# Optimization experiments

Hardware: AMD Instinct MI355X
Metric: run time of the kernel (lower is better)

## Reference

```python
import jax, jax.numpy as jnp
import numpy as np
import math

B, S, E = 2, 2048, 1024
H, HD = 16, 64
FF = 4 * E
EPS = float(jnp.finfo(jnp.float32).eps)  # torch nn.RMSNorm default eps


def setup_inputs() -> dict:
    key = jax.random.key(0)
    ks = jax.random.split(key, 20)
    sd = 0.02
    inp = {
        "x": jax.random.normal(ks[0], (B, S, E), jnp.float32),
        "wq": jax.random.normal(ks[1], (E, H * HD), jnp.float32) * sd,
        "bq": jnp.zeros((H * HD,), jnp.float32),
        "wk": jax.random.normal(ks[2], (E, HD), jnp.float32) * sd,
        "bk": jnp.zeros((HD,), jnp.float32),
        "wv": jax.random.normal(ks[3], (E, HD), jnp.float32) * sd,
        "bv": jnp.zeros((HD,), jnp.float32),
        "wo": jax.random.normal(ks[4], (H * HD, E), jnp.float32) * sd,
        "bo": jnp.zeros((E,), jnp.float32),
        "wg": jax.random.normal(ks[5], (E, FF), jnp.float32) * sd,
        "bg": jnp.zeros((FF,), jnp.float32),
        "wu": jax.random.normal(ks[6], (E, FF), jnp.float32) * sd,
        "bu": jnp.zeros((FF,), jnp.float32),
        "wd": jax.random.normal(ks[7], (FF, E), jnp.float32) * sd,
        "bd": jnp.zeros((E,), jnp.float32),
        "g1": jnp.ones((E,), jnp.float32),
        "g2": jnp.ones((E,), jnp.float32),
    }
    return inp


def rmsnorm(x, g):
    ms = jnp.mean(jnp.square(x), axis=-1, keepdims=True)
    return x * jax.lax.rsqrt(ms + EPS) * g


def apply_rope(t):
    # t: [B, H, S, D]; llama-style rotate-half, theta=10000, start_pos=0
    d = t.shape[-1]
    half = d // 2
    inv_freq = 1.0 / (10000.0 ** (jnp.arange(half, dtype=jnp.float32) / half))
    pos = jnp.arange(t.shape[2], dtype=jnp.float32)
    ang = pos[:, None] * inv_freq[None, :]  # [S, half]
    cos, sin = jnp.cos(ang), jnp.sin(ang)
    t1, t2 = t[..., :half], t[..., half:]
    return jnp.concatenate([t1 * cos - t2 * sin, t1 * sin + t2 * cos], axis=-1)


def decoder_fwd(x, wq, bq, wk, bk, wv, bv, wo, bo, wg, bg, wu, bu, wd, bd, g1, g2):
    residual = x
    h = rmsnorm(x, g1)
    # MQA projections: H query heads, 1 shared K/V head
    q = (h @ wq + bq).reshape(B, S, H, HD).transpose(0, 2, 1, 3)  # [B,H,S,D]
    k = (h @ wk + bk)[:, None]                                    # [B,1,S,D]
    v = (h @ wv + bv)                                             # [B,S,D]
    q = apply_rope(q)
    k = apply_rope(k)[:, 0]                                       # [B,S,D]
    scores = jnp.einsum("bhqd,bkd->bhqk", q, k) / math.sqrt(HD)
    causal = jnp.tril(jnp.ones((S, S), dtype=bool))
    scores = jnp.where(causal, scores, -jnp.inf)
    attn = jax.nn.softmax(scores, axis=-1)
    out = jnp.einsum("bhqk,bkd->bhqd", attn, v)
    out = out.transpose(0, 2, 1, 3).reshape(B, S, H * HD)
    x = (out @ wo + bo) + residual
    residual = x
    h = rmsnorm(x, g2)
    gated = jax.nn.gelu(h @ wg + bg, approximate=False)  # torch GELU is exact erf
    up = h @ wu + bu
    x = (up * gated) @ wd + bd
    return x + residual


def reference(x, wq, bq, wk, bk, wv, bv, wo, bo, wg, bg, wu, bu, wd, bd, g1, g2):
    return decoder_fwd(x, wq, bq, wk, bk, wv, bv, wo, bo, wg, bg, wu, bu, wd, bd, g1, g2)
```

## Files before the change

kernel.cpp:

```cpp
#include <hip/hip_runtime.h>
#include <hip/hip_bf16.h>
#include <math.h>

#define BB 2
#define SS 2048
#define EE 1024
#define HH 16
#define HD 64
#define FFF 4096
#define MROWS (BB * SS)
#define EPS_F 1.1920929e-7f
#define NQKV 1152

typedef __hip_bfloat16 bf16;
typedef __attribute__((ext_vector_type(8))) short short8;
typedef __attribute__((ext_vector_type(4))) short short4v;
typedef __attribute__((ext_vector_type(4))) float floatx4;

typedef const __attribute__((address_space(1))) void* gas_t;
typedef __attribute__((address_space(3))) void* las_t;

#define BAR __builtin_amdgcn_s_barrier()
#define WLG do { asm volatile("s_waitcnt lgkmcnt(0)" ::: "memory"); \
                 __builtin_amdgcn_sched_barrier(0); } while (0)
#define VMC(N) asm volatile("s_waitcnt vmcnt(" #N ")" ::: "memory")

__global__ __launch_bounds__(256) void rmsnorm_kernel(const float* __restrict__ x,
                                                      const float* __restrict__ g,
                                                      bf16* __restrict__ out,
                                                      int cols) {
    int row = blockIdx.x;
    const float* xr = x + (size_t)row * cols;
    float ss = 0.0f;
    for (int c = threadIdx.x; c < cols; c += 256) {
        float v = xr[c];
        ss += v * v;
    }
    for (int off = 32; off > 0; off >>= 1) ss += __shfl_xor(ss, off, 64);
    __shared__ float red[4];
    int wave = threadIdx.x >> 6;
    if ((threadIdx.x & 63) == 0) red[wave] = ss;
    __syncthreads();
    float tot = red[0] + red[1] + red[2] + red[3];
    float rs = rsqrtf(tot / (float)cols + EPS_F);
    bf16* orow = out + (size_t)row * cols;
    for (int c = threadIdx.x; c < cols; c += 256) {
        orow[c] = __float2bfloat16(xr[c] * rs * g[c]);
    }
}

__global__ __launch_bounds__(256) void transpose_cast_kernel(const float* __restrict__ W,
                                                             bf16* __restrict__ Wt,
                                                             int K, int N) {
    __shared__ float t[32][33];
    int n0 = blockIdx.x * 32, k0 = blockIdx.y * 32;
    int tx = threadIdx.x & 31, ty = threadIdx.x >> 5;
#pragma unroll
    for (int i = 0; i < 4; ++i) {
        int kk = ty + i * 8;
        t[kk][tx] = W[(size_t)(k0 + kk) * N + n0 + tx];
    }
    __syncthreads();
#pragma unroll
    for (int i = 0; i < 4; ++i) {
        int nn = ty + i * 8;
        Wt[(size_t)(n0 + nn) * K + k0 + tx] = __float2bfloat16(t[tx][nn]);
    }
}

__global__ __launch_bounds__(256) void pack_bqkv_kernel(const float* __restrict__ bq,
                                                        const float* __restrict__ bk,
                                                        const float* __restrict__ bv,
                                                        float* __restrict__ bqkv) {
    int t = blockIdx.x * 256 + threadIdx.x;
    if (t >= NQKV) return;
    float v;
    if (t < 1024)      v = bq[t];
    else if (t < 1088) v = bk[t - 1024];
    else               v = bv[t - 1088];
    bqkv[t] = v;
}

#define GK 64

__global__ __launch_bounds__(256) void gemm_qkv_kernel(
        const bf16* __restrict__ A, const bf16* __restrict__ Bt,
        const float* __restrict__ bias,
        bf16* __restrict__ qout, float* __restrict__ kvout, int K) {
    __shared__ short As[128 * GK];
    __shared__ short Bs[128 * GK];
    int tid = threadIdx.x;
    int wave = tid >> 6, lane = tid & 63;
    int wm = (wave >> 1) * 64, wn = (wave & 1) * 64;
    int row0 = blockIdx.y * 128, col0 = blockIdx.x * 128;
    int lr = lane & 15, lq = lane >> 4;

    int srow = wave * 32 + (lane >> 3);
    int scol = (lane & 7) * 8;
    const bf16* Abase = A + (size_t)(row0 + srow) * K + scol;
    const bf16* Bbase = Bt + (size_t)(col0 + srow) * K + scol;

    floatx4 acc[4][4];
#pragma unroll
    for (int mi = 0; mi < 4; ++mi)
#pragma unroll
        for (int ni = 0; ni < 4; ++ni)
            acc[mi][ni] = (floatx4){0.f, 0.f, 0.f, 0.f};

    for (int k0 = 0; k0 < K; k0 += GK) {
        __syncthreads();
#pragma unroll
        for (int c = 0; c < 4; ++c) {
            __builtin_amdgcn_global_load_lds(
                (gas_t)(Abase + (size_t)(c * 8) * K + k0),
                (las_t)&As[(wave * 32 + c * 8) * GK], 16, 0, 0);
            __builtin_amdgcn_global_load_lds(
                (gas_t)(Bbase + (size_t)(c * 8) * K + k0),
                (las_t)&Bs[(wave * 32 + c * 8) * GK], 16, 0, 0);
        }
        __syncthreads();
#pragma unroll
        for (int ks = 0; ks < GK; ks += 32) {
            short8 af[4], bfr[4];
#pragma unroll
            for (int mi = 0; mi < 4; ++mi)
                af[mi] = *(const short8*)&As[(wm + mi * 16 + lr) * GK + ks + lq * 8];
#pragma unroll
            for (int ni = 0; ni < 4; ++ni)
                bfr[ni] = *(const short8*)&Bs[(wn + ni * 16 + lr) * GK + ks + lq * 8];
#pragma unroll
            for (int mi = 0; mi < 4; ++mi)
#pragma unroll
                for (int ni = 0; ni < 4; ++ni)
                    acc[mi][ni] = __builtin_amdgcn_mfma_f32_16x16x32_bf16(
                        af[mi], bfr[ni], acc[mi][ni], 0, 0, 0);
        }
    }

#pragma unroll
    for (int mi = 0; mi < 4; ++mi) {
#pragma unroll
        for (int ni = 0; ni < 4; ++ni) {
            int gc = col0 + wn + ni * 16 + lr;
            float bv = bias[gc];
#pragma unroll
            for (int r = 0; r < 4; ++r) {
                int gr = row0 + wm + mi * 16 + lq * 4 + r;
                float c = acc[mi][ni][r] + bv;
                if (gc < 1024) qout[(size_t)gr * 1024 + gc] = __float2bfloat16(c);
                else           kvout[(size_t)gr * 128 + (gc - 1024)] = c;
            }
        }
    }
}

__global__ __launch_bounds__(256) void gemm_n128_kernel(
        const bf16* __restrict__ A, const bf16* __restrict__ Bt,
        const float* __restrict__ bias, const float* __restrict__ aux,
        float* __restrict__ C, int N, int K) {
    __shared__ short As[128 * GK];
    __shared__ short Bs[128 * GK];
    int tid = threadIdx.x;
    int wave = tid >> 6, lane = tid & 63;
    int wm = (wave >> 1) * 64, wn = (wave & 1) * 64;
    int row0 = blockIdx.y * 128, col0 = blockIdx.x * 128;
    int lr = lane & 15, lq = lane >> 4;

    int srow = wave * 32 + (lane >> 3);
    int scol = (lane & 7) * 8;
    const bf16* Abase = A + (size_t)(row0 + srow) * K + scol;
    const bf16* Bbase = Bt + (size_t)(col0 + srow) * K + scol;

    floatx4 acc[4][4];
#pragma unroll
    for (int mi = 0; mi < 4; ++mi)
#pragma unroll
        for (int ni = 0; ni < 4; ++ni)
            acc[mi][ni] = (floatx4){0.f, 0.f, 0.f, 0.f};

    for (int k0 = 0; k0 < K; k0 += GK) {
        __syncthreads();
#pragma unroll
        for (int c = 0; c < 4; ++c) {
            __builtin_amdgcn_global_load_lds(
                (gas_t)(Abase + (size_t)(c * 8) * K + k0),
                (las_t)&As[(wave * 32 + c * 8) * GK], 16, 0, 0);
            __builtin_amdgcn_global_load_lds(
                (gas_t)(Bbase + (size_t)(c * 8) * K + k0),
                (las_t)&Bs[(wave * 32 + c * 8) * GK], 16, 0, 0);
        }
        __syncthreads();
#pragma unroll
        for (int ks = 0; ks < GK; ks += 32) {
            short8 af[4], bfr[4];
#pragma unroll
            for (int mi = 0; mi < 4; ++mi)
                af[mi] = *(const short8*)&As[(wm + mi * 16 + lr) * GK + ks + lq * 8];
#pragma unroll
            for (int ni = 0; ni < 4; ++ni)
                bfr[ni] = *(const short8*)&Bs[(wn + ni * 16 + lr) * GK + ks + lq * 8];
#pragma unroll
            for (int mi = 0; mi < 4; ++mi)
#pragma unroll
                for (int ni = 0; ni < 4; ++ni)
                    acc[mi][ni] = __builtin_amdgcn_mfma_f32_16x16x32_bf16(
                        af[mi], bfr[ni], acc[mi][ni], 0, 0, 0);
        }
    }

#pragma unroll
    for (int mi = 0; mi < 4; ++mi) {
#pragma unroll
        for (int ni = 0; ni < 4; ++ni) {
            int gc = col0 + wn + ni * 16 + lr;
            float bv = bias[gc];
#pragma unroll
            for (int r = 0; r < 4; ++r) {
                int gr = row0 + wm + mi * 16 + lq * 4 + r;
                size_t idx = (size_t)gr * N + gc;
                C[idx] = acc[mi][ni][r] + bv + aux[idx];
            }
        }
    }
}

#define FFN_RD(KH, MH) \
    short8 af[4], gf[2], uf[2]; \
    { const short* Ap = &Ab[buf][KH][0]; const short* Bp = &Bb[buf][KH][0]; \
      af[0] = *(const short8*)&Ap[(wr * 128 + ((MH) * 4 + 0) * 16 + lr) * 32 + quad * 8]; \
      af[1] = *(const short8*)&Ap[(wr * 128 + ((MH) * 4 + 1) * 16 + lr) * 32 + quad * 8]; \
      af[2] = *(const short8*)&Ap[(wr * 128 + ((MH) * 4 + 2) * 16 + lr) * 32 + quad * 8]; \
      af[3] = *(const short8*)&Ap[(wr * 128 + ((MH) * 4 + 3) * 16 + lr) * 32 + quad * 8]; \
      gf[0] = *(const short8*)&Bp[(wc * 32 + lr) * 32 + quad * 8]; \
      gf[1] = *(const short8*)&Bp[(wc * 32 + 16 + lr) * 32 + quad * 8]; \
      uf[0] = *(const short8*)&Bp[4096 + (wc * 32 + lr) * 32 + quad * 8]; \
      uf[1] = *(const short8*)&Bp[4096 + (wc * 32 + 16 + lr) * 32 + quad * 8]; }

#define FFN_MM(MH) \
    __builtin_amdgcn_s_setprio(1); \
    { _Pragma("unroll") for (int mi = 0; mi < 4; ++mi) { \
        ag[(MH) * 4 + mi][0] = __builtin_amdgcn_mfma_f32_16x16x32_bf16(af[mi], gf[0], ag[(MH) * 4 + mi][0], 0, 0, 0); \
        ag[(MH) * 4 + mi][1] = __builtin_amdgcn_mfma_f32_16x16x32_bf16(af[mi], gf[1], ag[(MH) * 4 + mi][1], 0, 0, 0); \
        au[(MH) * 4 + mi][0] = __builtin_amdgcn_mfma_f32_16x16x32_bf16(af[mi], uf[0], au[(MH) * 4 + mi][0], 0, 0, 0); \
        au[(MH) * 4 + mi][1] = __builtin_amdgcn_mfma_f32_16x16x32_bf16(af[mi], uf[1], au[(MH) * 4 + mi][1], 0, 0, 0); } } \
    __builtin_amdgcn_s_setprio(0);

__global__ __launch_bounds__(512, 2) void gemm_ffn_kernel(
        const bf16* __restrict__ A, const bf16* __restrict__ Bg,
        const bf16* __restrict__ Bu, const float* __restrict__ biasg,
        const float* __restrict__ biasu, bf16* __restrict__ C, int K) {
    __shared__ short Ab[2][2][8192];
    __shared__ short Bb[2][2][8192];

    const int tid = threadIdx.x;
    const int w = tid >> 6, lane = tid & 63;
    const int wr = w >> 2, wc = w & 3;
    const int lr = lane & 15, quad = lane >> 4;
    const int row0 = blockIdx.y * 256, col0 = blockIdx.x * 128;
    const int NT = K >> 6;

    const int sr = tid >> 2;
    const int sc = (tid & 3) * 8;

    auto stageA = [&](short* dst, int kcol) {
        __builtin_amdgcn_global_load_lds(
            (gas_t)(A + (size_t)(row0 + sr) * K + kcol + sc),
            (las_t)(dst + tid * 8), 16, 0, 0);
        __builtin_amdgcn_global_load_lds(
            (gas_t)(A + (size_t)(row0 + 128 + sr) * K + kcol + sc),
            (las_t)(dst + 4096 + tid * 8), 16, 0, 0);
    };
    auto stageB = [&](short* dst, int kcol) {
        __builtin_amdgcn_global_load_lds(
            (gas_t)(Bg + (size_t)(col0 + sr) * K + kcol + sc),
            (las_t)(dst + tid * 8), 16, 0, 0);
        __builtin_amdgcn_global_load_lds(
            (gas_t)(Bu + (size_t)(col0 + sr) * K + kcol + sc),
            (las_t)(dst + 4096 + tid * 8), 16, 0, 0);
    };

    floatx4 ag[8][2], au[8][2];
#pragma unroll
    for (int mi = 0; mi < 8; ++mi)
#pragma unroll
        for (int ni = 0; ni < 2; ++ni) {
            ag[mi][ni] = (floatx4){0.f, 0.f, 0.f, 0.f};
            au[mi][ni] = (floatx4){0.f, 0.f, 0.f, 0.f};
        }

    stageA(&Ab[0][0][0], 0);
    stageB(&Bb[0][0][0], 0);
    stageA(&Ab[0][1][0], 32);
    stageB(&Bb[0][1][0], 32);
    stageA(&Ab[1][0][0], 64);
    stageB(&Bb[1][0][0], 64);
    VMC(8);
    BAR;

    for (int k = 0; k < NT; ++k) {
        const int buf = k & 1;
        {
            FFN_RD(0, 0)
            if (k + 1 < NT) stageA(&Ab[buf ^ 1][1][0], (k + 1) * 64 + 32);
            BAR; WLG;
            FFN_MM(0)
            BAR;
        }
        {
            FFN_RD(0, 1)
            if (k + 1 < NT) stageB(&Bb[buf ^ 1][1][0], (k + 1) * 64 + 32);
            BAR; WLG;
            FFN_MM(1)
            if (k < NT - 1) { VMC(8); } else { VMC(0); }
            BAR;
        }
        {
            FFN_RD(1, 0)
            if (k + 2 < NT) stageA(&Ab[buf][0][0], (k + 2) * 64);
            BAR; WLG;
            FFN_MM(0)
            BAR;
        }
        {
            FFN_RD(1, 1)
            if (k + 2 < NT) stageB(&Bb[buf][0][0], (k + 2) * 64);
            BAR; WLG;
            FFN_MM(1)
            if (k < NT - 2) { VMC(8); } else if (k == NT - 2) { VMC(4); }
            BAR;
        }
    }

#pragma unroll
    for (int mi = 0; mi < 8; ++mi) {
#pragma unroll
        for (int ni = 0; ni < 2; ++ni) {
            int gc = col0 + wc * 32 + ni * 16 + lr;
            float bg_ = biasg[gc], bu_ = biasu[gc];
#pragma unroll
            for (int r = 0; r < 4; ++r) {
                int gr = row0 + wr * 128 + mi * 16 + quad * 4 + r;
                float g = ag[mi][ni][r] + bg_;
                float u = au[mi][ni][r] + bu_;
                float v = 0.5f * g * (1.0f + erff(g * 0.70710678118654752f)) * u;
                C[(size_t)gr * FFF + gc] = __float2bfloat16(v);
            }
        }
    }
}

__global__ __launch_bounds__(256) void rope_table_kernel(float* __restrict__ ct,
                                                         float* __restrict__ st) {
    int idx = blockIdx.x * 256 + threadIdx.x;
    int i = idx & 31, s = idx >> 5;
    float inv = powf(10000.0f, -(float)i / 32.0f);
    float ang = (float)s * inv;
    ct[idx] = cosf(ang);
    st[idx] = sinf(ang);
}

__global__ __launch_bounds__(256) void rope_q_kernel(bf16* __restrict__ t,
                                                     const float* __restrict__ ct,
                                                     const float* __restrict__ st,
                                                     int total) {
    int idx = blockIdx.x * 256 + threadIdx.x;
    if (idx >= total) return;
    int i = idx & 31;
    int h = (idx >> 5) % HH;
    int row = idx / (32 * HH);
    int s = row & (SS - 1);
    float c = ct[s * 32 + i];
    float sn = st[s * 32 + i];
    size_t base = (size_t)row * (HH * HD) + h * 64 + i;
    float t1 = (float)t[base];
    float t2 = (float)t[base + 32];
    t[base]      = __float2bfloat16((t1 * c - t2 * sn) * 0.125f);
    t[base + 32] = __float2bfloat16((t1 * sn + t2 * c) * 0.125f);
}

__global__ __launch_bounds__(256) void prep_kv_kernel(const float* __restrict__ kv,
                                                      const float* __restrict__ ct,
                                                      const float* __restrict__ st,
                                                      bf16* __restrict__ kbf,
                                                      bf16* __restrict__ vtb) {
    __shared__ float vt[64][65];
    int s0 = blockIdx.x * 64;
    int b  = blockIdx.y;
    int tid = threadIdx.x;

    for (int i = tid; i < 2048; i += 256) {
        int sl = i >> 5, ii = i & 31;
        int s = s0 + sl;
        size_t base = ((size_t)(b * SS + s)) * 128;
        float k1 = kv[base + ii], k2 = kv[base + ii + 32];
        float c = ct[s * 32 + ii];
        float sn = st[s * 32 + ii];
        size_t ob = ((size_t)(b * SS + s)) * 64;
        kbf[ob + ii]      = __float2bfloat16(k1 * c - k2 * sn);
        kbf[ob + ii + 32] = __float2bfloat16(k1 * sn + k2 * c);
    }

    for (int i = tid; i < 4096; i += 256) {
        int s = i >> 6, d = i & 63;
        vt[d][s] = kv[((size_t)(b * SS + s0 + s)) * 128 + 64 + d];
    }
    __syncthreads();
    for (int i = tid; i < 4096; i += 256) {
        int d = i >> 6, sl = i & 63;
        vtb[((size_t)(b * 64 + d)) * SS + s0 + sl] = __float2bfloat16(vt[d][sl]);
    }
}

#define PST 68
#define SM_SHIFT 6.0f

__global__ __launch_bounds__(256, 3) void attn_mfma_kernel(
        const bf16* __restrict__ q, const bf16* __restrict__ kb,
        const bf16* __restrict__ vt,
        float* __restrict__ O0p, float* __restrict__ O1p,
        float* __restrict__ l0p, float* __restrict__ l1p) {
    __shared__ short Kb_s[2][64 * 64];
    __shared__ short Vb_s[2][64 * 64];
    __shared__ short Ps[4][16 * PST];

    int h = blockIdx.y, b = blockIdx.z;
    int px = blockIdx.x >> 1, half = blockIdx.x & 1;
    int tid = threadIdx.x, w = tid >> 6, lane = tid & 63;
    int lr = lane & 15, quad = lane >> 4;
    int rsw = lane & 7;

    float* __restrict__ Op = half ? O1p : O0p;
    float* __restrict__ lp = half ? l1p : l0p;

    const bf16* kbB = kb + (size_t)b * SS * 64;
    const bf16* vtB = vt + (size_t)b * 64 * SS;

    int st_sub = lane >> 3;
    int st_col = ((lane & 7) ^ st_sub) << 3;

    auto stage_tile = [&](int nxt, int j0s) {
#pragma unroll
        for (int i = 0; i < 2; ++i) {
            int rr = i * 32 + w * 8 + st_sub;
            __builtin_amdgcn_global_load_lds(
                (gas_t)(kbB + (size_t)(j0s + rr) * 64 + st_col),
                (las_t)&Kb_s[nxt][(i * 256 + w * 64) * 8], 16, 0, 0);
            __builtin_amdgcn_global_load_lds(
                (gas_t)(vtB + (size_t)rr * SS + j0s + st_col),
                (las_t)&Vb_s[nxt][(i * 256 + w * 64) * 8], 16, 0, 0);
        }
    };

    for (int pass = 0; pass < 2; ++pass) {
        int qt = (pass == 0) ? px : (SS / 64 - 1 - px);
        int q0 = qt * 64;

        const bf16* qrow = q + ((size_t)(b * SS + q0 + w * 16 + lr)) * (HH * HD) + h * HD;
        short8 qf0 = *(const short8*)(qrow + quad * 8);
        short8 qf1 = *(const short8*)(qrow + 32 + quad * 8);

        int n  = qt + 1;
        int n0 = (n + 1) >> 1;
        int tlo = half ? n0 : 0;
        int thi = half ? n  : n0;

        floatx4 O[4];
#pragma unroll
        for (int ni = 0; ni < 4; ++ni) O[ni] = (floatx4){0.f, 0.f, 0.f, 0.f};
        float lrow[4] = {0.f, 0.f, 0.f, 0.f};

        int cur = 0;
        if (tlo < thi) stage_tile(0, tlo * 64);
        __syncthreads();

        for (int t = tlo; t < thi; ++t) {
            if (t + 1 < thi) stage_tile(cur ^ 1, (t + 1) * 64);

            int j0 = t * 64;

            floatx4 S[4];
#pragma unroll
            for (int ni = 0; ni < 4; ++ni) S[ni] = (floatx4){0.f, 0.f, 0.f, 0.f};
#pragma unroll
            for (int ni = 0; ni < 4; ++ni) {
                const short* Kc = &Kb_s[cur][(ni * 16 + lr) * 64];
                short8 b0 = *(const short8*)&Kc[(quad ^ rsw) * 8];
                short8 b1 = *(const short8*)&Kc[((quad ^ rsw) ^ 4) * 8];
                S[ni] = __builtin_amdgcn_mfma_f32_16x16x32_bf16(qf0, b0, S[ni], 0, 0, 0);
                S[ni] = __builtin_amdgcn_mfma_f32_16x16x32_bf16(qf1, b1, S[ni], 0, 0, 0);
            }

            short8 vf[8];
#pragma unroll
            for (int ni = 0; ni < 4; ++ni) {
                const short* Vc = &Vb_s[cur][(ni * 16 + lr) * 64];
                vf[2 * ni]     = *(const short8*)&Vc[(quad ^ rsw) * 8];
                vf[2 * ni + 1] = *(const short8*)&Vc[((quad ^ rsw) ^ 4) * 8];
            }

            if (t == qt) {
                int rowg = q0 + w * 16 + quad * 4;
#pragma unroll
                for (int ni = 0; ni < 4; ++ni) {
                    int colg = j0 + ni * 16 + lr;
#pragma unroll
                    for (int r = 0; r < 4; ++r)
                        if (colg > rowg + r) S[ni][r] = -3.0e38f;
                }
            }

#pragma unroll
            for (int ni = 0; ni < 4; ++ni)
#pragma unroll
                for (int r = 0; r < 4; ++r)
                    S[ni][r] = __expf(S[ni][r] - SM_SHIFT);
#pragma unroll
            for (int r = 0; r < 4; ++r)
                lrow[r] += S[0][r] + S[1][r] + S[2][r] + S[3][r];

#pragma unroll
            for (int ni = 0; ni < 4; ++ni)
#pragma unroll
                for (int r = 0; r < 4; ++r) {
                    bf16 pb = __float2bfloat16(S[ni][r]);
                    Ps[w][(quad * 4 + r) * PST + ni * 16 + lr] = *(short*)&pb;
                }
            short4v a0 = *(const short4v*)&Ps[w][lr * PST + quad * 8];
            short4v a1 = *(const short4v*)&Ps[w][lr * PST + quad * 8 + 4];
            short4v a2 = *(const short4v*)&Ps[w][lr * PST + 32 + quad * 8];
            short4v a3 = *(const short4v*)&Ps[w][lr * PST + 32 + quad * 8 + 4];
            short8 p0 = __builtin_shufflevector(a0, a1, 0, 1, 2, 3, 4, 5, 6, 7);
            short8 p1 = __builtin_shufflevector(a2, a3, 0, 1, 2, 3, 4, 5, 6, 7);

#pragma unroll
            for (int ni = 0; ni < 4; ++ni) {
                O[ni] = __builtin_amdgcn_mfma_f32_16x16x32_bf16(p0, vf[2 * ni], O[ni], 0, 0, 0);
                O[ni] = __builtin_amdgcn_mfma_f32_16x16x32_bf16(p1, vf[2 * ni + 1], O[ni], 0, 0, 0);
            }

            __syncthreads();
            cur ^= 1;
        }

#pragma unroll
        for (int r = 0; r < 4; ++r) {
            float l = lrow[r];
            for (int off = 1; off < 16; off <<= 1) l += __shfl_xor(l, off, 64);
            lrow[r] = l;
        }

#pragma unroll
        for (int ni = 0; ni < 4; ++ni) {
            int gc = h * 64 + ni * 16 + lr;
#pragma unroll
            for (int r = 0; r < 4; ++r) {
                int gr = b * SS + q0 + w * 16 + quad * 4 + r;
                Op[(size_t)gr * (HH * HD) + gc] = O[ni][r];
            }
        }
        if (lr == 0) {
#pragma unroll
            for (int r = 0; r < 4; ++r) {
                int gr = b * SS + q0 + w * 16 + quad * 4 + r;
                lp[(size_t)gr * HH + h] = lrow[r];
            }
        }
    }
}

__global__ __launch_bounds__(256) void attn_combine_kernel(
        const float* __restrict__ O0p, const float* __restrict__ O1p,
        const float* __restrict__ l0p, const float* __restrict__ l1p,
        bf16* __restrict__ o) {
    int idx = blockIdx.x * 256 + threadIdx.x;
    int d4  = idx & 15;
    int hh  = (idx >> 4) & 15;
    int row = idx >> 8;
    float l = l0p[row * HH + hh] + l1p[row * HH + hh];
    float inv = 1.0f / l;
    size_t base = (size_t)row * (HH * HD) + hh * 64 + d4 * 4;
    float4 a = *(const float4*)(O0p + base);
    float4 c = *(const float4*)(O1p + base);
    short4v o4;
    {
        bf16 v0 = __float2bfloat16((a.x + c.x) * inv);
        bf16 v1 = __float2bfloat16((a.y + c.y) * inv);
        bf16 v2 = __float2bfloat16((a.z + c.z) * inv);
        bf16 v3 = __float2bfloat16((a.w + c.w) * inv);
        o4[0] = *(short*)&v0; o4[1] = *(short*)&v1;
        o4[2] = *(short*)&v2; o4[3] = *(short*)&v3;
    }
    *(short4v*)(o + base) = o4;
}

#define MB (1024ull * 1024ull)

extern "C" void kernel_launch(void* const* d_in, const int* in_sizes, int n_in,
                              void* d_out, int out_size, void* d_ws, size_t ws_size,
                              hipStream_t stream) {
    const float* x  = (const float*)d_in[0];
    const float* wq = (const float*)d_in[1];
    const float* bq = (const float*)d_in[2];
    const float* wk = (const float*)d_in[3];
    const float* bk = (const float*)d_in[4];
    const float* wv = (const float*)d_in[5];
    const float* bv = (const float*)d_in[6];
    const float* wo = (const float*)d_in[7];
    const float* bo = (const float*)d_in[8];
    const float* wg = (const float*)d_in[9];
    const float* bg = (const float*)d_in[10];
    const float* wu = (const float*)d_in[11];
    const float* bu = (const float*)d_in[12];
    const float* wd = (const float*)d_in[13];
    const float* bd = (const float*)d_in[14];
    const float* g1 = (const float*)d_in[15];
    const float* g2 = (const float*)d_in[16];
    float* out = (float*)d_out;

    char* ws = (char*)d_ws;
    bf16*  qbf   = (bf16*)(ws);
    bf16*  wuT   = (bf16*)(ws + 8 * MB);
    float* x2    = (float*)(ws + 16 * MB);
    bf16*  h1b   = (bf16*)(ws + 32 * MB);
    float* kv    = (float*)(ws + 40 * MB);
    bf16*  ao    = (bf16*)(ws + 42 * MB);
    bf16*  gg    = (bf16*)(ws + 50 * MB);
    bf16*  kbf   = (bf16*)(ws + 50 * MB);
    bf16*  vtb   = (bf16*)(ws + 50 * MB + 512 * 1024);
    float* Opart0 = (float*)(ws + 16 * MB);
    float* Opart1 = (float*)(ws + 51 * MB);
    float* lpart0 = (float*)(ws + 67 * MB);
    float* lpart1 = (float*)(ws + 67 * MB + 256 * 1024);
    float* ctab   = (float*)(ws + 68 * MB);
    float* stab   = (float*)(ws + 68 * MB + 256 * 1024);
    bf16*  wqkvT = (bf16*)(ws + 82 * MB);
    float* bqkv  = (float*)(ws + 84 * MB + 512 * 1024);
    bf16*  woT   = (bf16*)(ws + 85 * MB);
    bf16*  wgT   = (bf16*)(ws);
    bf16*  wdT   = (bf16*)(ws + 42 * MB);
    bf16*  h2b   = h1b;

    rmsnorm_kernel<<<MROWS, 256, 0, stream>>>(x, g1, h1b, EE);

    transpose_cast_kernel<<<dim3(EE / 32, EE / 32), 256, 0, stream>>>(wq, wqkvT, EE, EE);
    transpose_cast_kernel<<<dim3(HD / 32, EE / 32), 256, 0, stream>>>(wk, wqkvT + (size_t)1024 * EE, EE, HD);
    transpose_cast_kernel<<<dim3(HD / 32, EE / 32), 256, 0, stream>>>(wv, wqkvT + (size_t)1088 * EE, EE, HD);
    pack_bqkv_kernel<<<(NQKV + 255) / 256, 256, 0, stream>>>(bq, bk, bv, bqkv);
    transpose_cast_kernel<<<dim3(EE / 32, EE / 32), 256, 0, stream>>>(wo, woT, EE, EE);

    gemm_qkv_kernel<<<dim3(NQKV / 128, MROWS / 128), 256, 0, stream>>>(
        h1b, wqkvT, bqkv, qbf, kv, EE);

    rope_table_kernel<<<(SS * 32) / 256, 256, 0, stream>>>(ctab, stab);

    {
        int total_q = MROWS * HH * 32;
        rope_q_kernel<<<(total_q + 255) / 256, 256, 0, stream>>>(qbf, ctab, stab, total_q);
    }
    prep_kv_kernel<<<dim3(SS / 64, BB), 256, 0, stream>>>(kv, ctab, stab, kbf, vtb);

    attn_mfma_kernel<<<dim3(2 * SS / 128, HH, BB), 256, 0, stream>>>(
        qbf, kbf, vtb, Opart0, Opart1, lpart0, lpart1);
    attn_combine_kernel<<<(MROWS * HH * HD / 4) / 256, 256, 0, stream>>>(
        Opart0, Opart1, lpart0, lpart1, ao);

    gemm_n128_kernel<<<dim3(EE / 128, MROWS / 128), 256, 0, stream>>>(
        ao, woT, bo, x, x2, EE, EE);

    rmsnorm_kernel<<<MROWS, 256, 0, stream>>>(x2, g2, h2b, EE);

    transpose_cast_kernel<<<dim3(FFF / 32, EE / 32), 256, 0, stream>>>(wg, wgT, EE, FFF);
    transpose_cast_kernel<<<dim3(FFF / 32, EE / 32), 256, 0, stream>>>(wu, wuT, EE, FFF);

    gemm_ffn_kernel<<<dim3(FFF / 128, MROWS / 256), 512, 0, stream>>>(
        h2b, wgT, wuT, bg, bu, gg, EE);

    transpose_cast_kernel<<<dim3(EE / 32, FFF / 32), 256, 0, stream>>>(wd, wdT, FFF, EE);
    gemm_n128_kernel<<<dim3(EE / 128, MROWS / 128), 256, 0, stream>>>(
        gg, wdT, bd, x2, out, EE, FFF);
}
```

Measured before the change: 461.4 us.

## Shrink N=1024 GEMM tiles to 128x64 and swizzle FFN LDS layout

The output-projection and down-projection GEMMs now use 128x64 tiles with each wave owning 32 rows, which doubles the block count (512 blocks instead of 256) so the GPU's compute units stay busier. The FFN gate/up kernel gets an XOR swizzle on its LDS column index to reduce bank conflicts on fragment reads. It also loads the B fragments once per K-half and reuses them across both M-halves instead of reloading them. The smaller tiles lower arithmetic intensity and add global traffic in exchange for more parallelism.

```diff
diff --git a/kernel.cpp b/kernel.cpp
--- a/kernel.cpp
+++ b/kernel.cpp
@@ -154,26 +154,26 @@
     }
 }
 
-__global__ __launch_bounds__(256) void gemm_n128_kernel(
+__global__ __launch_bounds__(256) void gemm_n64_kernel(
         const bf16* __restrict__ A, const bf16* __restrict__ Bt,
         const float* __restrict__ bias, const float* __restrict__ aux,
-        float* __restrict__ C, int N, int K) {
+        float* __restrict__ C, int M, int N, int K) {
     __shared__ short As[128 * GK];
-    __shared__ short Bs[128 * GK];
+    __shared__ short Bs[64 * GK];
     int tid = threadIdx.x;
     int wave = tid >> 6, lane = tid & 63;
-    int wm = (wave >> 1) * 64, wn = (wave & 1) * 64;
-    int row0 = blockIdx.y * 128, col0 = blockIdx.x * 128;
+    int wm = wave * 32;
+    int row0 = blockIdx.y * 128, col0 = blockIdx.x * 64;
     int lr = lane & 15, lq = lane >> 4;
 
-    int srow = wave * 32 + (lane >> 3);
+    int srow = (lane >> 3);
     int scol = (lane & 7) * 8;
-    const bf16* Abase = A + (size_t)(row0 + srow) * K + scol;
-    const bf16* Bbase = Bt + (size_t)(col0 + srow) * K + scol;
-
-    floatx4 acc[4][4];
-#pragma unroll
-    for (int mi = 0; mi < 4; ++mi)
+    const bf16* Abase = A + (size_t)(row0 + wave * 32 + srow) * K + scol;
+    const bf16* Bbase = Bt + (size_t)(col0 + wave * 16 + srow) * K + scol;
+
+    floatx4 acc[2][4];
+#pragma unroll
+    for (int mi = 0; mi < 2; ++mi)
 #pragma unroll
         for (int ni = 0; ni < 4; ++ni)
             acc[mi][ni] = (floatx4){0.f, 0.f, 0.f, 0.f};
@@ -181,26 +181,27 @@
     for (int k0 = 0; k0 < K; k0 += GK) {
         __syncthreads();
 #pragma unroll
-        for (int c = 0; c < 4; ++c) {
+        for (int c = 0; c < 4; ++c)
             __builtin_amdgcn_global_load_lds(
                 (gas_t)(Abase + (size_t)(c * 8) * K + k0),
                 (las_t)&As[(wave * 32 + c * 8) * GK], 16, 0, 0);
+#pragma unroll
+        for (int c = 0; c < 2; ++c)
             __builtin_amdgcn_global_load_lds(
                 (gas_t)(Bbase + (size_t)(c * 8) * K + k0),
-                (las_t)&Bs[(wave * 32 + c * 8) * GK], 16, 0, 0);
-        }
+                (las_t)&Bs[(wave * 16 + c * 8) * GK], 16, 0, 0);
         __syncthreads();
 #pragma unroll
         for (int ks = 0; ks < GK; ks += 32) {
-            short8 af[4], bfr[4];
-#pragma unroll
-            for (int mi = 0; mi < 4; ++mi)
+            short8 af[2], bfr[4];
+#pragma unroll
+            for (int mi = 0; mi < 2; ++mi)
                 af[mi] = *(const short8*)&As[(wm + mi * 16 + lr) * GK + ks + lq * 8];
 #pragma unroll
             for (int ni = 0; ni < 4; ++ni)
-                bfr[ni] = *(const short8*)&Bs[(wn + ni * 16 + lr) * GK + ks + lq * 8];
-#pragma unroll
-            for (int mi = 0; mi < 4; ++mi)
+                bfr[ni] = *(const short8*)&Bs[(ni * 16 + lr) * GK + ks + lq * 8];
+#pragma unroll
+            for (int mi = 0; mi < 2; ++mi)
 #pragma unroll
                 for (int ni = 0; ni < 4; ++ni)
                     acc[mi][ni] = __builtin_amdgcn_mfma_f32_16x16x32_bf16(
@@ -209,10 +210,10 @@
     }
 
 #pragma unroll
-    for (int mi = 0; mi < 4; ++mi) {
+    for (int mi = 0; mi < 2; ++mi) {
 #pragma unroll
         for (int ni = 0; ni < 4; ++ni) {
-            int gc = col0 + wn + ni * 16 + lr;
+            int gc = col0 + ni * 16 + lr;
             float bv = bias[gc];
 #pragma unroll
             for (int r = 0; r < 4; ++r) {
@@ -224,17 +225,19 @@
     }
 }
 
-#define FFN_RD(KH, MH) \
-    short8 af[4], gf[2], uf[2]; \
-    { const short* Ap = &Ab[buf][KH][0]; const short* Bp = &Bb[buf][KH][0]; \
-      af[0] = *(const short8*)&Ap[(wr * 128 + ((MH) * 4 + 0) * 16 + lr) * 32 + quad * 8]; \
-      af[1] = *(const short8*)&Ap[(wr * 128 + ((MH) * 4 + 1) * 16 + lr) * 32 + quad * 8]; \
-      af[2] = *(const short8*)&Ap[(wr * 128 + ((MH) * 4 + 2) * 16 + lr) * 32 + quad * 8]; \
-      af[3] = *(const short8*)&Ap[(wr * 128 + ((MH) * 4 + 3) * 16 + lr) * 32 + quad * 8]; \
-      gf[0] = *(const short8*)&Bp[(wc * 32 + lr) * 32 + quad * 8]; \
-      gf[1] = *(const short8*)&Bp[(wc * 32 + 16 + lr) * 32 + quad * 8]; \
-      uf[0] = *(const short8*)&Bp[4096 + (wc * 32 + lr) * 32 + quad * 8]; \
-      uf[1] = *(const short8*)&Bp[4096 + (wc * 32 + 16 + lr) * 32 + quad * 8]; }
+#define FFN_RD_A(KH, MH) \
+    { const short* Ap = &Ab[buf][KH][0]; \
+      af[0] = *(const short8*)&Ap[(wr * 128 + ((MH) * 4 + 0) * 16 + lr) * 32 + cs8]; \
+      af[1] = *(const short8*)&Ap[(wr * 128 + ((MH) * 4 + 1) * 16 + lr) * 32 + cs8]; \
+      af[2] = *(const short8*)&Ap[(wr * 128 + ((MH) * 4 + 2) * 16 + lr) * 32 + cs8]; \
+      af[3] = *(const short8*)&Ap[(wr * 128 + ((MH) * 4 + 3) * 16 + lr) * 32 + cs8]; }
+
+#define FFN_RD_B(KH) \
+    { const short* Bp = &Bb[buf][KH][0]; \
+      gf[0] = *(const short8*)&Bp[(wc * 32 + lr) * 32 + cs8]; \
+      gf[1] = *(const short8*)&Bp[(wc * 32 + 16 + lr) * 32 + cs8]; \
+      uf[0] = *(const short8*)&Bp[4096 + (wc * 32 + lr) * 32 + cs8]; \
+      uf[1] = *(const short8*)&Bp[4096 + (wc * 32 + 16 + lr) * 32 + cs8]; }
 
 #define FFN_MM(MH) \
     __builtin_amdgcn_s_setprio(1); \
@@ -258,24 +261,25 @@
     const int lr = lane & 15, quad = lane >> 4;
     const int row0 = blockIdx.y * 256, col0 = blockIdx.x * 128;
     const int NT = K >> 6;
+    const int cs8 = (quad ^ ((lr >> 1) & 3)) * 8;
 
     const int sr = tid >> 2;
-    const int sc = (tid & 3) * 8;
+    const int scs = (((tid & 3) ^ ((tid >> 3) & 3))) * 8;
 
     auto stageA = [&](short* dst, int kcol) {
         __builtin_amdgcn_global_load_lds(
-            (gas_t)(A + (size_t)(row0 + sr) * K + kcol + sc),
+            (gas_t)(A + (size_t)(row0 + sr) * K + kcol + scs),
             (las_t)(dst + tid * 8), 16, 0, 0);
         __builtin_amdgcn_global_load_lds(
-            (gas_t)(A + (size_t)(row0 + 128 + sr) * K + kcol + sc),
+            (gas_t)(A + (size_t)(row0 + 128 + sr) * K + kcol + scs),
             (las_t)(dst + 4096 + tid * 8), 16, 0, 0);
     };
     auto stageB = [&](short* dst, int kcol) {
         __builtin_amdgcn_global_load_lds(
-            (gas_t)(Bg + (size_t)(col0 + sr) * K + kcol + sc),
+            (gas_t)(Bg + (size_t)(col0 + sr) * K + kcol + scs),
             (las_t)(dst + tid * 8), 16, 0, 0);
         __builtin_amdgcn_global_load_lds(
-            (gas_t)(Bu + (size_t)(col0 + sr) * K + kcol + sc),
+            (gas_t)(Bu + (size_t)(col0 + sr) * K + kcol + scs),
             (las_t)(dst + 4096 + tid * 8), 16, 0, 0);
     };
 
@@ -299,15 +303,19 @@
 
     for (int k = 0; k < NT; ++k) {
         const int buf = k & 1;
+        short8 gf[2], uf[2];
         {
-            FFN_RD(0, 0)
+            short8 af[4];
+            FFN_RD_A(0, 0)
+            FFN_RD_B(0)
             if (k + 1 < NT) stageA(&Ab[buf ^ 1][1][0], (k + 1) * 64 + 32);
             BAR; WLG;
             FFN_MM(0)
             BAR;
         }
         {
-            FFN_RD(0, 1)
+            short8 af[4];
+            FFN_RD_A(0, 1)
             if (k + 1 < NT) stageB(&Bb[buf ^ 1][1][0], (k + 1) * 64 + 32);
             BAR; WLG;
             FFN_MM(1)
@@ -315,14 +323,17 @@
             BAR;
         }
         {
-            FFN_RD(1, 0)
+            short8 af[4];
+            FFN_RD_A(1, 0)
+            FFN_RD_B(1)
             if (k + 2 < NT) stageA(&Ab[buf][0][0], (k + 2) * 64);
             BAR; WLG;
             FFN_MM(0)
             BAR;
         }
         {
-            FFN_RD(1, 1)
+            short8 af[4];
+            FFN_RD_A(1, 1)
             if (k + 2 < NT) stageB(&Bb[buf][0][0], (k + 2) * 64);
             BAR; WLG;
             FFN_MM(1)
@@ -664,8 +675,8 @@
     attn_combine_kernel<<<(MROWS * HH * HD / 4) / 256, 256, 0, stream>>>(
         Opart0, Opart1, lpart0, lpart1, ao);
 
-    gemm_n128_kernel<<<dim3(EE / 128, MROWS / 128), 256, 0, stream>>>(
-        ao, woT, bo, x, x2, EE, EE);
+    gemm_n64_kernel<<<dim3(EE / 64, MROWS / 128), 256, 0, stream>>>(
+        ao, woT, bo, x, x2, MROWS, EE, EE);
 
     rmsnorm_kernel<<<MROWS, 256, 0, stream>>>(x2, g2, h2b, EE);
 
@@ -676,6 +687,6 @@
         h2b, wgT, wuT, bg, bu, gg, EE);
 
     transpose_cast_kernel<<<dim3(EE / 32, FFF / 32), 256, 0, stream>>>(wd, wdT, FFF, EE);
-    gemm_n128_kernel<<<dim3(EE / 128, MROWS / 128), 256, 0, stream>>>(
-        gg, wdT, bd, x2, out, EE, FFF);
-}
+    gemm_n64_kernel<<<dim3(EE / 64, MROWS / 128), 256, 0, stream>>>(
+        gg, wdT, bd, x2, out, MROWS, EE, FFF);
+}
```

After: 429.0 us. -7.0%, faster.
